# Kernel optimization log

Hardware: AMD Instinct MI355X
Metric: run time of the kernel (lower is better)

Reference implementation:

```python
import jax, jax.numpy as jnp
import numpy as np

D_MODEL = 3072
N_HEADS = 24
HEAD_DIM = D_MODEL // N_HEADS          # 128
Q_PROJ = D_MODEL // 2                  # 1536
KV_PROJ = 2 * D_MODEL // 3             # 2048
ROPE_DIM = HEAD_DIM // 2               # 64 (qk_rope_dim == qk_no_rope_dim)
MAX_LEN = 2048
ROPE_THETA = 10000.0
EPS = 1e-6
B, S = 2, 2048


def setup_inputs() -> dict:
    key = jax.random.key(0)
    ks = jax.random.split(key, 7)
    return {
        "x": jax.random.normal(ks[0], (B, S, D_MODEL), dtype=jnp.float32),
        "scale": jnp.ones((D_MODEL,), dtype=jnp.float32),
        "w_dq": 0.01 * jax.random.normal(ks[1], (D_MODEL, Q_PROJ), dtype=jnp.float32),
        "w_uq": 0.01 * jax.random.normal(ks[2], (Q_PROJ, D_MODEL), dtype=jnp.float32),
        "w_dkv": 0.01 * jax.random.normal(ks[3], (D_MODEL, KV_PROJ + ROPE_DIM), dtype=jnp.float32),
        "w_ukv": 0.01 * jax.random.normal(ks[4], (KV_PROJ, D_MODEL + N_HEADS * ROPE_DIM), dtype=jnp.float32),
        "w_o": 0.01 * jax.random.normal(ks[5], (D_MODEL, D_MODEL), dtype=jnp.float32),
    }


def _rope_cos_sin(seq_len):
    # freqs over full head_dim, sliced to rope_dim//2 then tiled x2 (as in torch repeat)
    freqs = 1.0 / (ROPE_THETA ** (jnp.arange(0, HEAD_DIM, 2, dtype=jnp.float32) / HEAD_DIM))
    angles = jnp.arange(seq_len, dtype=jnp.float32)[:, None] * freqs[None, :]  # [S, 64]
    ang = angles[:, : ROPE_DIM // 2]                                            # [S, 32]
    cos = jnp.tile(jnp.cos(ang), (1, 2))                                        # [S, 64]
    sin = jnp.tile(jnp.sin(ang), (1, 2))
    return cos[None, None], sin[None, None]  # [1,1,S,64]


def _rotate_half(t):
    a, b = jnp.split(t, 2, axis=-1)
    return jnp.concatenate([-b, a], axis=-1)


def reference(x, scale, w_dq, w_uq, w_dkv, w_ukv, w_o):
    b, s, _ = x.shape
    # RMSNorm pre-normalization
    xn = scale * (x * jax.lax.rsqrt(jnp.mean(x * x, axis=-1, keepdims=True) + EPS))
    # two-stage query projection
    q = (xn @ w_dq) @ w_uq                                   # [B,S,D]
    q = q.reshape(b, s, N_HEADS, HEAD_DIM).transpose(0, 2, 1, 3)  # [B,H,S,hd]
    q_no_rope, q_rope = jnp.split(q, [ROPE_DIM], axis=-1)
    cos, sin = _rope_cos_sin(s)
    q_rope = q_rope * cos + _rotate_half(q_rope) * sin
    # KV down projection (this is the kv cache)
    kv_down = xn @ w_dkv                                     # [B,S,KV_PROJ+rope]
    kv_no_rope, k_rope = jnp.split(kv_down, [KV_PROJ], axis=-1)
    # KV up projection
    kv_up = kv_no_rope @ w_ukv                               # [B,S,H*(hd+rope)]
    kv_up = kv_up.reshape(b, s, N_HEADS, HEAD_DIM + ROPE_DIM).transpose(0, 2, 1, 3)
    key, value = jnp.split(kv_up, [ROPE_DIM], axis=-1)       # key [B,H,S,64], value [B,H,S,128]
    # shared rope key (one head, broadcast to all heads)
    k_rope = k_rope[:, None, :, :]                           # [B,1,S,64]
    k_rope = k_rope * cos + _rotate_half(k_rope) * sin
    k_rope = jnp.broadcast_to(k_rope, (b, N_HEADS, s, ROPE_DIM))
    final_q = jnp.concatenate([q_no_rope, q_rope], axis=-1)  # [B,H,S,128]
    final_k = jnp.concatenate([key, k_rope], axis=-1)        # [B,H,S,128]
    # masked SDPA (causal, past_length=0)
    inv_scale = 1.0 / jnp.sqrt(jnp.asarray(HEAD_DIM, dtype=x.dtype))
    scores = jnp.einsum("bhsd,bhtd->bhst", final_q, final_k) * inv_scale
    causal = jnp.tril(jnp.ones((s, s), dtype=bool))
    scores = jnp.where(causal[None, None], scores, jnp.asarray(-1e30, dtype=scores.dtype))
    attn = jax.nn.softmax(scores, axis=-1)
    attn_out = jnp.einsum("bhst,bhtd->bhsd", attn, value)    # [B,H,S,128]
    attn_out = attn_out.transpose(0, 2, 1, 3).reshape(b, s, D_MODEL)
    output = attn_out @ w_o.T
    return output, kv_down
```

## Files before the change

### kernel.cpp

```cpp
#include <hip/hip_runtime.h>
#include <hip/hip_bf16.h>
#include <stdint.h>

using bf16_t = __bf16;
using bf16x8 = __attribute__((ext_vector_type(8))) __bf16;
using bf16x4 = __attribute__((ext_vector_type(4))) __bf16;
using f32x4  = __attribute__((ext_vector_type(4))) float;

#define D_MODEL 3072
#define N_HEADS 24
#define HEAD_DIM 128
#define Q_PROJ 1536
#define KV_PROJ 2048
#define ROPE_DIM 64
#define S_LEN 2048
#define NTOK 4096
#define KVDN 2112
#define KVUN 4608

__device__ __forceinline__ void async_ld16(const void* g, void* l) {
    __builtin_amdgcn_global_load_lds(
        (__attribute__((address_space(1))) uint32_t*)(uintptr_t)g,
        (__attribute__((address_space(3))) uint32_t*)(uint32_t)(uintptr_t)l,
        16, 0, 0);
}

#define BARRIER() __builtin_amdgcn_s_barrier()
#define WAITVN(n) asm volatile("s_waitcnt vmcnt(" #n ")" ::: "memory")

__global__ __launch_bounds__(256) void rmsnorm_kernel(
    const float* __restrict__ x, const float* __restrict__ sc, bf16_t* __restrict__ xn)
{
    const int tok = blockIdx.x;
    const int t = threadIdx.x;
    const float4* xr = (const float4*)(x + (size_t)tok * D_MODEL);
    float4 a = xr[t], b = xr[t + 256], c = xr[t + 512];
    float ss = a.x*a.x + a.y*a.y + a.z*a.z + a.w*a.w
             + b.x*b.x + b.y*b.y + b.z*b.z + b.w*b.w
             + c.x*c.x + c.y*c.y + c.z*c.z + c.w*c.w;
    #pragma unroll
    for (int off = 32; off >= 1; off >>= 1) ss += __shfl_xor(ss, off);
    __shared__ float red[4];
    if ((t & 63) == 0) red[t >> 6] = ss;
    __syncthreads();
    const float inv = rsqrtf((red[0] + red[1] + red[2] + red[3]) * (1.0f / D_MODEL) + 1e-6f);
    const float4* sr = (const float4*)sc;
    float4 s0 = sr[t], s1 = sr[t + 256], s2 = sr[t + 512];
    bf16x4* xo = (bf16x4*)(xn + (size_t)tok * D_MODEL);
    bf16x4 o;
    o[0]=(bf16_t)(a.x*s0.x*inv); o[1]=(bf16_t)(a.y*s0.y*inv); o[2]=(bf16_t)(a.z*s0.z*inv); o[3]=(bf16_t)(a.w*s0.w*inv);
    xo[t] = o;
    o[0]=(bf16_t)(b.x*s1.x*inv); o[1]=(bf16_t)(b.y*s1.y*inv); o[2]=(bf16_t)(b.z*s1.z*inv); o[3]=(bf16_t)(b.w*s1.w*inv);
    xo[t + 256] = o;
    o[0]=(bf16_t)(c.x*s2.x*inv); o[1]=(bf16_t)(c.y*s2.y*inv); o[2]=(bf16_t)(c.z*s2.z*inv); o[3]=(bf16_t)(c.w*s2.w*inv);
    xo[t + 512] = o;
}

__global__ void transpose_conv(const float* __restrict__ in, bf16_t* __restrict__ out, int K, int N)
{
    __shared__ float tile[32][33];
    const int n0 = blockIdx.x * 32, k0 = blockIdx.y * 32;
    const int tx = threadIdx.x, ty = threadIdx.y;
    #pragma unroll
    for (int i = 0; i < 32; i += 8)
        tile[ty + i][tx] = in[(size_t)(k0 + ty + i) * N + n0 + tx];
    __syncthreads();
    #pragma unroll
    for (int i = 0; i < 32; i += 8)
        out[(size_t)(n0 + ty + i) * K + k0 + tx] = (bf16_t)tile[tx][ty + i];
}

__global__ void conv_bf16(const float* __restrict__ in, bf16_t* __restrict__ out, int n4)
{
    const int stride = gridDim.x * 256;
    for (int i = blockIdx.x * 256 + threadIdx.x; i < n4; i += stride) {
        float4 v = ((const float4*)in)[i];
        bf16x4 o;
        o[0] = (bf16_t)v.x; o[1] = (bf16_t)v.y; o[2] = (bf16_t)v.z; o[3] = (bf16_t)v.w;
        ((bf16x4*)out)[i] = o;
    }
}

template<int RH, int BNF>
__device__ __forceinline__ void mfmaQ(f32x4 (&acc)[8][BNF], const bf16x8 (&af)[4],
                                      const bf16x8 (&bfv)[BNF]) {
    __builtin_amdgcn_s_setprio(1);
    #pragma unroll
    for (int i = 0; i < 4; ++i)
        #pragma unroll
        for (int cf = 0; cf < BNF; ++cf)
            acc[RH*4+i][cf] = __builtin_amdgcn_mfma_f32_16x16x32_bf16(af[i], bfv[cf], acc[RH*4+i][cf], 0, 0, 0);
    __builtin_amdgcn_s_setprio(0);
}

template<int BNF>
__global__ __launch_bounds__(512, 2) void gemm256(
    const bf16_t* __restrict__ A, const bf16_t* __restrict__ B, int N, int K,
    float* __restrict__ Cf, int ldf, int flo, int fhi,
    bf16_t* __restrict__ Cb1, int ldb1, int b1lo, int b1hi,
    bf16_t* __restrict__ Cb2, int ldb2, int b2lo, int b2hi,
    bf16_t* __restrict__ vt, float cbscale)
{
    constexpr int BN = BNF * 64;
    constexpr uint32_t BSLOT = BNF * 4096;
    __shared__ char LDS[65536 + 4 * BSLOT];
    char* Lc = LDS;
    const int tid = threadIdx.x;
    const int wv = tid >> 6, lane = tid & 63;
    const int fr = lane & 15, fg = lane >> 4;
    const int wr = wv >> 2, wc = wv & 3;
    const bool bwave = (wv < 2 * BNF);

    int lin = blockIdx.y * gridDim.x + blockIdx.x;
    const int nwg = gridDim.x * gridDim.y;
    if ((nwg & 7) == 0) lin = (lin & 7) * (nwg >> 3) + (lin >> 3);
    const int bx = lin % gridDim.x, by = lin / gridDim.x;
    const int m0 = by << 8, n0 = bx * BN;

    const uint32_t slot4 = (uint32_t)((fg ^ ((fr >> 1) & 3)) << 4);

    const bf16_t* agp[2]; const bf16_t* bgp[2];
    uint32_t aoff[2], boff[2];
    #pragma unroll
    for (int j = 0; j < 2; ++j) {
        const int c = j * 512 + tid;
        const int g = c ^ ((c >> 3) & 3);
        agp[j] = A + (size_t)(m0 + (g >> 2)) * K + (g & 3) * 8;
        aoff[j] = (uint32_t)((j * 8 + wv) * 1024);
        const int cb = j * (BNF * 128) + tid;
        const int gb = cb ^ ((cb >> 3) & 3);
        int br = n0 + (gb >> 2); if (br > N - 1) br = N - 1;
        bgp[j] = B + (size_t)br * K + (gb & 3) * 8;
        boff[j] = (uint32_t)(j * (BNF * 2048) + wv * 1024);
    }

    f32x4 acc[8][BNF];
    f32x4 zero = {0.f, 0.f, 0.f, 0.f};
    #pragma unroll
    for (int i = 0; i < 8; ++i)
        #pragma unroll
        for (int j = 0; j < BNF; ++j) acc[i][j] = zero;

    bf16x8 A0[4], A1[4], B0[BNF], B1[BNF];
    const int rowA = (wr << 7) + fr;
    const int rowB = wc * (BNF * 16) + fr;

    auto stA = [&](int t, int kh) {
        const uint32_t sb = (uint32_t)(((2*t + kh) & 3) << 14);
        #pragma unroll
        for (int j = 0; j < 2; ++j)
            async_ld16(agp[j] + t * 64 + kh * 32, Lc + sb + aoff[j]);
    };
    auto stB = [&](int t, int kh) {
        const uint32_t sb = 65536u + (uint32_t)(((2*t + kh) & 3) * BSLOT);
        if (tid < BNF * 128) {
            #pragma unroll
            for (int j = 0; j < 2; ++j)
                async_ld16(bgp[j] + t * 64 + kh * 32, Lc + sb + boff[j]);
        }
    };
    auto ldA4 = [&](int t, int kh, int rh, bf16x8 (&dst)[4]) {
        const uint32_t base = (uint32_t)(((2*t + kh) & 3) << 14);
        #pragma unroll
        for (int i = 0; i < 4; ++i)
            dst[i] = *(const bf16x8*)(Lc + base + (rowA + (rh * 4 + i) * 16) * 64 + slot4);
    };
    auto ldBn = [&](int t, int kh, bf16x8 (&dst)[BNF]) {
        const uint32_t base = 65536u + (uint32_t)(((2*t + kh) & 3) * BSLOT);
        #pragma unroll
        for (int cf = 0; cf < BNF; ++cf)
            dst[cf] = *(const bf16x8*)(Lc + base + (rowB + cf * 16) * 64 + slot4);
    };

    const int NT = K >> 6;
    stA(0, 0); stB(0, 0); stA(0, 1); stB(0, 1);
    stA(1, 0); stB(1, 0); stA(1, 1); stB(1, 1);
    if (bwave) { WAITVN(8); } else { WAITVN(4); }
    BARRIER();
    ldA4(0, 0, 0, A0); ldBn(0, 0, B0);

    for (int t = 0; t < NT; ++t) {
        const bool pref = (t + 2 < NT);
        ldA4(t, 0, 1, A1);
        mfmaQ<0, BNF>(acc, A0, B0);
        if (pref) { if (bwave) { WAITVN(4); } else { WAITVN(2); } }
        else      { WAITVN(0); }
        BARRIER();
        ldA4(t, 1, 0, A0); ldBn(t, 1, B1);
        if (pref) { stA(t + 2, 0); stB(t + 2, 0); }
        mfmaQ<1, BNF>(acc, A1, B0);
        BARRIER();
        ldA4(t, 1, 1, A1);
        mfmaQ<0, BNF>(acc, A0, B1);
        BARRIER();
        if (t + 1 < NT) { ldA4(t + 1, 0, 0, A0); ldBn(t + 1, 0, B0); }
        if (pref) { stA(t + 2, 1); stB(t + 2, 1); }
        mfmaQ<1, BNF>(acc, A1, B1);
        BARRIER();
    }

    const int colb = n0 + wc * (BNF * 16) + fr;
    const int rowb = m0 + (wr << 7) + fg * 4;
    if (vt) {
        #pragma unroll
        for (int rf = 0; rf < 8; ++rf) {
            const int row0 = rowb + rf * 16;
            const int bb = row0 >> 11, s0 = row0 & 2047;
            #pragma unroll
            for (int cf = 0; cf < BNF; ++cf) {
                const int col = colb + cf * 16;
                const int h = col / 192;
                const int dm = col - h * 192;
                if (dm < 64) {
                    #pragma unroll
                    for (int r = 0; r < 4; ++r)
                        Cb1[(size_t)(row0 + r) * ldb1 + col] = (bf16_t)acc[rf][cf][r];
                } else {
                    bf16x4 o;
                    o[0] = (bf16_t)acc[rf][cf][0];
                    o[1] = (bf16_t)acc[rf][cf][1];
                    o[2] = (bf16_t)acc[rf][cf][2];
                    o[3] = (bf16_t)acc[rf][cf][3];
                    *(bf16x4*)(vt + ((size_t)((bb * 24 + h) * 128 + dm - 64)) * 2048 + s0) = o;
                }
            }
        }
    } else {
        #pragma unroll
        for (int rf = 0; rf < 8; ++rf)
            #pragma unroll
            for (int cf = 0; cf < BNF; ++cf) {
                const int col = colb + cf * 16;
                #pragma unroll
                for (int r = 0; r < 4; ++r) {
                    const int row = rowb + rf * 16 + r;
                    const float v = acc[rf][cf][r];
                    if (Cf  && col >= flo  && col < fhi)  Cf [(size_t)row * ldf  + col - flo]  = v;
                    if (Cb1 && col >= b1lo && col < b1hi) Cb1[(size_t)row * ldb1 + col - b1lo] = (bf16_t)(v * cbscale);
                    if (Cb2 && col >= b2lo && col < b2hi) Cb2[(size_t)row * ldb2 + col - b2lo] = (bf16_t)v;
                }
            }
    }
}

__global__ void rope_tab(float* __restrict__ ctab, float* __restrict__ stab)
{
    const int idx = blockIdx.x * 256 + threadIdx.x;
    if (idx >= S_LEN * 32) return;
    const int s = idx >> 5, i = idx & 31;
    const float freq = powf(10000.0f, -(float)(2 * i) * (1.0f / 128.0f));
    const float ang = (float)s * freq;
    ctab[idx] = cosf(ang);
    stab[idx] = sinf(ang);
}

__global__ void rope_q_kernel(bf16_t* __restrict__ q, const float* __restrict__ ctab,
                              const float* __restrict__ stab)
{
    const int idx = blockIdx.x * 256 + threadIdx.x;
    if (idx >= NTOK * N_HEADS * 32) return;
    const int i = idx & 31;
    const int rest = idx >> 5;
    const int h = rest % N_HEADS;
    const int tok = rest / N_HEADS;
    const int s = tok & (S_LEN - 1);
    bf16_t* p = q + (size_t)tok * D_MODEL + h * HEAD_DIM + 64;
    const float a = (float)p[i], b = (float)p[i + 32];
    const float c = ctab[s * 32 + i], sn = stab[s * 32 + i];
    p[i]      = (bf16_t)(a * c - b * sn);
    p[i + 32] = (bf16_t)(b * c + a * sn);
}

__global__ void rope_k_kernel(const float* __restrict__ kvd, bf16_t* __restrict__ kr,
                              const float* __restrict__ ctab, const float* __restrict__ stab)
{
    const int idx = blockIdx.x * 256 + threadIdx.x;
    if (idx >= NTOK * 32) return;
    const int i = idx & 31;
    const int tok = idx >> 5;
    const int s = tok & (S_LEN - 1);
    const float* p = kvd + (size_t)tok * KVDN + KV_PROJ;
    const float a = p[i], b = p[i + 32];
    const float c = ctab[s * 32 + i], sn = stab[s * 32 + i];
    kr[(size_t)tok * 64 + i]      = (bf16_t)(a * c - b * sn);
    kr[(size_t)tok * 64 + i + 32] = (bf16_t)(b * c + a * sn);
}

__global__ __launch_bounds__(256, 2) void attn_fwd(
    const bf16_t* __restrict__ Q, const bf16_t* __restrict__ KVUP,
    const bf16_t* __restrict__ KR, const bf16_t* __restrict__ VT,
    bf16_t* __restrict__ AO)
{
    __shared__ bf16_t Knr[2][64 * 64];
    __shared__ bf16_t Krp[2][64 * 64];
    __shared__ bf16_t Vls[2][128 * 64];

    const int bh = blockIdx.y;
    const int b = bh / N_HEADS, h = bh % N_HEADS;
    const int wave = threadIdx.x >> 6, lane = threadIdx.x & 63;
    const int fr = lane & 15, fg = lane >> 4;
    const int rx = fr & 7;
    const int hi = fg >> 1;
    const int s0l = fr + 32 * (fg & 1);
    const int s1l = s0l + 16;

    const bf16_t* Kb  = KVUP + (size_t)b * S_LEN * KVUN + (size_t)h * 192;
    const bf16_t* KRb = KR + (size_t)b * S_LEN * 64;
    const bf16_t* Vb  = VT + (size_t)bh * HEAD_DIM * S_LEN;

    const int srow   = lane >> 3;
    const int schunk = (lane & 7) ^ srow;

    f32x4 zero = {0.f, 0.f, 0.f, 0.f};

    #pragma unroll 1
    for (int tp = 0; tp < 2; ++tp) {
        const int qt = (tp == 0) ? blockIdx.x : (15 - blockIdx.x);
        const int qb = qt * 128;
        const int wrow0 = qb + wave * 32;

        bf16x8 qf[2][4];
        #pragma unroll
        for (int rf = 0; rf < 2; ++rf)
            #pragma unroll
            for (int kc = 0; kc < 4; ++kc)
                qf[rf][kc] = *(const bf16x8*)(Q + (size_t)(b * S_LEN + wrow0 + rf * 16 + fr) * D_MODEL
                                              + h * HEAD_DIM + kc * 32 + fg * 8);
        f32x4 oacc[2][8];
        float m_i[2], l_i[2];
        #pragma unroll
        for (int rf = 0; rf < 2; ++rf) {
            #pragma unroll
            for (int nf = 0; nf < 8; ++nf) oacc[rf][nf] = zero;
            m_i[rf] = -1e30f; l_i[rf] = 0.f;
        }

        auto stage = [&](int kvb, int bf) {
            #pragma unroll
            for (int c = 0; c < 2; ++c) {
                const int r0 = wave * 16 + c * 8;
                async_ld16(Kb  + (size_t)(kvb + r0 + srow) * KVUN + schunk * 8, &Knr[bf][r0 * 64]);
                async_ld16(KRb + (size_t)(kvb + r0 + srow) * 64   + schunk * 8, &Krp[bf][r0 * 64]);
            }
            #pragma unroll
            for (int c = 0; c < 4; ++c) {
                const int r0 = wave * 32 + c * 8;
                async_ld16(Vb + (size_t)(r0 + srow) * S_LEN + kvb + schunk * 8, &Vls[bf][r0 * 64]);
            }
        };

        const int kvend = qb + 128;
        int cur = 0;
        stage(0, 0);
        __syncthreads();

        #pragma unroll 1
        for (int kvb = 0; kvb < kvend; kvb += 64) {
            if (kvb + 64 < kvend) stage(kvb + 64, cur ^ 1);

            if (kvb <= wrow0 + 31) {
                const bf16_t* Kc = Knr[cur];
                const bf16_t* Rc = Krp[cur];
                const bf16_t* Vc = Vls[cur];

                f32x4 sacc[2][4];
                #pragma unroll
                for (int rf = 0; rf < 2; ++rf)
                    #pragma unroll
                    for (int jn = 0; jn < 4; ++jn) sacc[rf][jn] = zero;
                __builtin_amdgcn_s_setprio(1);
                #pragma unroll
                for (int jn = 0; jn < 4; ++jn) {
                    const int krow = jn * 16 + fr;
                    bf16x8 kA = *(const bf16x8*)(Kc + krow * 64 + (((0 + fg) ^ rx) << 3));
                    bf16x8 kB = *(const bf16x8*)(Kc + krow * 64 + (((4 + fg) ^ rx) << 3));
                    bf16x8 kC = *(const bf16x8*)(Rc + krow * 64 + (((0 + fg) ^ rx) << 3));
                    bf16x8 kD = *(const bf16x8*)(Rc + krow * 64 + (((4 + fg) ^ rx) << 3));
                    #pragma unroll
                    for (int rf = 0; rf < 2; ++rf) {
                        sacc[rf][jn] = __builtin_amdgcn_mfma_f32_16x16x32_bf16(kA, qf[rf][0], sacc[rf][jn], 0, 0, 0);
                        sacc[rf][jn] = __builtin_amdgcn_mfma_f32_16x16x32_bf16(kB, qf[rf][1], sacc[rf][jn], 0, 0, 0);
                        sacc[rf][jn] = __builtin_amdgcn_mfma_f32_16x16x32_bf16(kC, qf[rf][2], sacc[rf][jn], 0, 0, 0);
                        sacc[rf][jn] = __builtin_amdgcn_mfma_f32_16x16x32_bf16(kD, qf[rf][3], sacc[rf][jn], 0, 0, 0);
                    }
                }
                __builtin_amdgcn_s_setprio(0);

                const bool needMask = (kvb + 63 > wrow0);
                uint32_t pk[2][4][2];
                #pragma unroll
                for (int rf = 0; rf < 2; ++rf) {
                    const int qrow = wrow0 + rf * 16 + fr;
                    float mx = -1e30f;
                    #pragma unroll
                    for (int jn = 0; jn < 4; ++jn)
                        #pragma unroll
                        for (int r = 0; r < 4; ++r) {
                            float v = sacc[rf][jn][r];
                            if (needMask && (kvb + jn * 16 + fg * 4 + r > qrow)) v = -1e30f;
                            sacc[rf][jn][r] = v;
                            mx = fmaxf(mx, v);
                        }
                    mx = fmaxf(mx, __shfl_xor(mx, 16));
                    mx = fmaxf(mx, __shfl_xor(mx, 32));
                    if (!__all(mx <= m_i[rf] + 8.f)) {
                        const float mn = fmaxf(m_i[rf], mx);
                        const float sc = __builtin_amdgcn_exp2f(m_i[rf] - mn);
                        m_i[rf] = mn;
                        l_i[rf] *= sc;
                        #pragma unroll
                        for (int nf = 0; nf < 8; ++nf)
                            #pragma unroll
                            for (int r = 0; r < 4; ++r) oacc[rf][nf][r] *= sc;
                    }
                    const float mn = m_i[rf];
                    float ls = 0.f;
                    #pragma unroll
                    for (int jn = 0; jn < 4; ++jn) {
                        float p0 = __builtin_amdgcn_exp2f(sacc[rf][jn][0] - mn);
                        float p1 = __builtin_amdgcn_exp2f(sacc[rf][jn][1] - mn);
                        float p2 = __builtin_amdgcn_exp2f(sacc[rf][jn][2] - mn);
                        float p3 = __builtin_amdgcn_exp2f(sacc[rf][jn][3] - mn);
                        ls += (p0 + p1) + (p2 + p3);
                        union { bf16x4 h; uint32_t w[2]; } cv;
                        cv.h[0] = (bf16_t)p0; cv.h[1] = (bf16_t)p1;
                        cv.h[2] = (bf16_t)p2; cv.h[3] = (bf16_t)p3;
                        pk[rf][jn][0] = cv.w[0]; pk[rf][jn][1] = cv.w[1];
                    }
                    ls += __shfl_xor(ls, 16);
                    ls += __shfl_xor(ls, 32);
                    l_i[rf] += ls;
                }

                bf16x8 bfr[2][2];
                #pragma unroll
                for (int rf = 0; rf < 2; ++rf)
                    #pragma unroll
                    for (int ks = 0; ks < 2; ++ks) {
                        const uint32_t t00 = __shfl(pk[rf][2*ks][0],   s0l);
                        const uint32_t t01 = __shfl(pk[rf][2*ks][1],   s0l);
                        const uint32_t t10 = __shfl(pk[rf][2*ks+1][0], s0l);
                        const uint32_t t11 = __shfl(pk[rf][2*ks+1][1], s0l);
                        const uint32_t u00 = __shfl(pk[rf][2*ks][0],   s1l);
                        const uint32_t u01 = __shfl(pk[rf][2*ks][1],   s1l);
                        const uint32_t u10 = __shfl(pk[rf][2*ks+1][0], s1l);
                        const uint32_t u11 = __shfl(pk[rf][2*ks+1][1], s1l);
                        union { bf16x8 h; uint32_t w[4]; } bb;
                        bb.w[0] = hi ? t10 : t00;
                        bb.w[1] = hi ? t11 : t01;
                        bb.w[2] = hi ? u10 : u00;
                        bb.w[3] = hi ? u11 : u01;
                        bfr[rf][ks] = bb.h;
                    }

                __builtin_amdgcn_s_setprio(1);
                #pragma unroll
                for (int nf = 0; nf < 8; ++nf) {
                    const int vrow = nf * 16 + fr;
                    bf16x8 v0 = *(const bf16x8*)(Vc + vrow * 64 + (((0 + fg) ^ rx) << 3));
                    bf16x8 v1 = *(const bf16x8*)(Vc + vrow * 64 + (((4 + fg) ^ rx) << 3));
                    #pragma unroll
                    for (int rf = 0; rf < 2; ++rf) {
                        oacc[rf][nf] = __builtin_amdgcn_mfma_f32_16x16x32_bf16(v0, bfr[rf][0], oacc[rf][nf], 0, 0, 0);
                        oacc[rf][nf] = __builtin_amdgcn_mfma_f32_16x16x32_bf16(v1, bfr[rf][1], oacc[rf][nf], 0, 0, 0);
                    }
                }
                __builtin_amdgcn_s_setprio(0);
            }
            __syncthreads();
            cur ^= 1;
        }

        #pragma unroll
        for (int rf = 0; rf < 2; ++rf) {
            const float rl = __builtin_amdgcn_rcpf(l_i[rf]);
            const int qrow = wrow0 + rf * 16 + fr;
            bf16_t* aob = AO + (size_t)(b * S_LEN + qrow) * D_MODEL + h * HEAD_DIM + fg * 4;
            #pragma unroll
            for (int nf = 0; nf < 8; ++nf) {
                bf16x4 o;
                o[0] = (bf16_t)(oacc[rf][nf][0] * rl);
                o[1] = (bf16_t)(oacc[rf][nf][1] * rl);
                o[2] = (bf16_t)(oacc[rf][nf][2] * rl);
                o[3] = (bf16_t)(oacc[rf][nf][3] * rl);
                *(bf16x4*)(aob + nf * 16) = o;
            }
        }
    }
}

extern "C" void kernel_launch(void* const* d_in, const int* in_sizes, int n_in,
                              void* d_out, int out_size, void* d_ws, size_t ws_size,
                              hipStream_t stream)
{
    const float* x     = (const float*)d_in[0];
    const float* scale = (const float*)d_in[1];
    const float* w_dq  = (const float*)d_in[2];
    const float* w_uq  = (const float*)d_in[3];
    const float* w_dkv = (const float*)d_in[4];
    const float* w_ukv = (const float*)d_in[5];
    const float* w_o   = (const float*)d_in[6];
    float* out0 = (float*)d_out;
    float* out1 = out0 + (size_t)NTOK * D_MODEL;

    if (ws_size < 187039744ull) return;
    char* ws = (char*)d_ws;
    bf16_t* XN    = (bf16_t*)(ws + 0);
    bf16_t* WCAT  = (bf16_t*)(ws + 25165824ull);
    bf16_t* WUQT  = (bf16_t*)(ws + 47579136ull);
    bf16_t* WUKVT = (bf16_t*)(ws + 57016320ull);
    bf16_t* WOB   = (bf16_t*)(ws + 75890688ull);
    bf16_t* QD    = (bf16_t*)(ws + 94765056ull);
    bf16_t* Qb    = (bf16_t*)(ws + 107347968ull);
    bf16_t* KVNR  = (bf16_t*)(ws + 132513792ull);
    bf16_t* KVUP  = (bf16_t*)(ws + 149291008ull);
    bf16_t* KRB   = (bf16_t*)(ws + 94765056ull);
    float*  CTAB  = (float*) (ws + 95289344ull);
    float*  STAB  = (float*) (ws + 95551488ull);
    bf16_t* VTb   = WCAT;
    bf16_t* AO    = XN;

    const float l2e_isc = 0.127500625f;

    rmsnorm_kernel<<<NTOK, 256, 0, stream>>>(x, scale, XN);
    transpose_conv<<<dim3(1536/32, 3072/32), dim3(32,8), 0, stream>>>(w_dq,  WCAT, 3072, 1536);
    transpose_conv<<<dim3(2112/32, 3072/32), dim3(32,8), 0, stream>>>(w_dkv, WCAT + (size_t)1536*3072, 3072, 2112);
    transpose_conv<<<dim3(3072/32, 1536/32), dim3(32,8), 0, stream>>>(w_uq,  WUQT, 1536, 3072);
    transpose_conv<<<dim3(4608/32, 2048/32), dim3(32,8), 0, stream>>>(w_ukv, WUKVT, 2048, 4608);
    conv_bf16<<<2048, 256, 0, stream>>>(w_o, WOB, (D_MODEL * D_MODEL) / 4);

    gemm256<4><<<dim3(15, 16), 512, 0, stream>>>(XN, WCAT, 3648, 3072,
        out1, KVDN, 1536, 3648,
        QD,   Q_PROJ, 0, 1536,
        KVNR, KV_PROJ, 1536, 3584, nullptr, 1.0f);
    gemm256<3><<<dim3(16, 16), 512, 0, stream>>>(QD, WUQT, 3072, 1536,
        nullptr, 0, 0, 0, Qb, D_MODEL, 0, 3072, nullptr, 0, 0, 0, nullptr, l2e_isc);
    rope_tab<<<(S_LEN * 32 + 255) / 256, 256, 0, stream>>>(CTAB, STAB);
    rope_q_kernel<<<(NTOK * N_HEADS * 32 + 255) / 256, 256, 0, stream>>>(Qb, CTAB, STAB);
    rope_k_kernel<<<(NTOK * 32 + 255) / 256, 256, 0, stream>>>(out1, KRB, CTAB, STAB);
    gemm256<3><<<dim3(24, 16), 512, 0, stream>>>(KVNR, WUKVT, 4608, 2048,
        nullptr, 0, 0, 0, KVUP, KVUN, 0, 0, nullptr, 0, 0, 0, VTb, 1.0f);
    attn_fwd<<<dim3(8, 48), 256, 0, stream>>>(Qb, KVUP, KRB, VTb, AO);
    gemm256<3><<<dim3(16, 16), 512, 0, stream>>>(AO, WOB, 3072, 3072,
        out0, D_MODEL, 0, 3072, nullptr, 0, 0, 0, nullptr, 0, 0, 0, nullptr, 1.0f);
}
```

Baseline: 521.7 us.

## Drop LDS staging in attention; load K/V fragments directly from global per wave

The attention kernel no longer stages K, rope-K and V tiles into double-buffered shared memory with async loads and block barriers. Each wave now reads its MFMA operands straight from global memory (through the cache) and runs only up to its own causal end, so the __syncthreads and LDS traffic go away. Launch bounds are raised to 4 blocks per CU. The trade-off is that the four waves of a block, which share the same K/V rows, each fetch them from global/L2 separately, and there is no explicit prefetch overlap, so load latency sits on the critical path.

```diff
diff --git a/kernel.cpp b/kernel.cpp
--- a/kernel.cpp
+++ b/kernel.cpp
@@ -286,20 +286,15 @@
     kr[(size_t)tok * 64 + i + 32] = (bf16_t)(b * c + a * sn);
 }
 
-__global__ __launch_bounds__(256, 2) void attn_fwd(
+__global__ __launch_bounds__(256, 4) void attn_fwd(
     const bf16_t* __restrict__ Q, const bf16_t* __restrict__ KVUP,
     const bf16_t* __restrict__ KR, const bf16_t* __restrict__ VT,
     bf16_t* __restrict__ AO)
 {
-    __shared__ bf16_t Knr[2][64 * 64];
-    __shared__ bf16_t Krp[2][64 * 64];
-    __shared__ bf16_t Vls[2][128 * 64];
-
     const int bh = blockIdx.y;
     const int b = bh / N_HEADS, h = bh % N_HEADS;
     const int wave = threadIdx.x >> 6, lane = threadIdx.x & 63;
     const int fr = lane & 15, fg = lane >> 4;
-    const int rx = fr & 7;
     const int hi = fg >> 1;
     const int s0l = fr + 32 * (fg & 1);
     const int s1l = s0l + 16;
@@ -307,9 +302,6 @@
     const bf16_t* Kb  = KVUP + (size_t)b * S_LEN * KVUN + (size_t)h * 192;
     const bf16_t* KRb = KR + (size_t)b * S_LEN * 64;
     const bf16_t* Vb  = VT + (size_t)bh * HEAD_DIM * S_LEN;
-
-    const int srow   = lane >> 3;
-    const int schunk = (lane & 7) ^ srow;
 
     f32x4 zero = {0.f, 0.f, 0.f, 0.f};
 
@@ -335,140 +327,114 @@
             m_i[rf] = -1e30f; l_i[rf] = 0.f;
         }
 
-        auto stage = [&](int kvb, int bf) {
-            #pragma unroll
-            for (int c = 0; c < 2; ++c) {
-                const int r0 = wave * 16 + c * 8;
-                async_ld16(Kb  + (size_t)(kvb + r0 + srow) * KVUN + schunk * 8, &Knr[bf][r0 * 64]);
-                async_ld16(KRb + (size_t)(kvb + r0 + srow) * 64   + schunk * 8, &Krp[bf][r0 * 64]);
+        const int kvend_w = wrow0 + 32;
+        #pragma unroll 1
+        for (int kvb = 0; kvb < kvend_w; kvb += 64) {
+            f32x4 sacc[2][4];
+            #pragma unroll
+            for (int rf = 0; rf < 2; ++rf)
+                #pragma unroll
+                for (int jn = 0; jn < 4; ++jn) sacc[rf][jn] = zero;
+            __builtin_amdgcn_s_setprio(1);
+            #pragma unroll
+            for (int jn = 0; jn < 4; ++jn) {
+                const int krow = kvb + jn * 16 + fr;
+                const bf16_t* kp = Kb + (size_t)krow * KVUN + fg * 8;
+                const bf16_t* rp = KRb + (size_t)krow * 64 + fg * 8;
+                bf16x8 kA = *(const bf16x8*)(kp);
+                bf16x8 kB = *(const bf16x8*)(kp + 32);
+                bf16x8 kC = *(const bf16x8*)(rp);
+                bf16x8 kD = *(const bf16x8*)(rp + 32);
+                #pragma unroll
+                for (int rf = 0; rf < 2; ++rf) {
+                    sacc[rf][jn] = __builtin_amdgcn_mfma_f32_16x16x32_bf16(kA, qf[rf][0], sacc[rf][jn], 0, 0, 0);
+                    sacc[rf][jn] = __builtin_amdgcn_mfma_f32_16x16x32_bf16(kB, qf[rf][1], sacc[rf][jn], 0, 0, 0);
+                    sacc[rf][jn] = __builtin_amdgcn_mfma_f32_16x16x32_bf16(kC, qf[rf][2], sacc[rf][jn], 0, 0, 0);
+                    sacc[rf][jn] = __builtin_amdgcn_mfma_f32_16x16x32_bf16(kD, qf[rf][3], sacc[rf][jn], 0, 0, 0);
+                }
             }
-            #pragma unroll
-            for (int c = 0; c < 4; ++c) {
-                const int r0 = wave * 32 + c * 8;
-                async_ld16(Vb + (size_t)(r0 + srow) * S_LEN + kvb + schunk * 8, &Vls[bf][r0 * 64]);
+            __builtin_amdgcn_s_setprio(0);
+
+            const bool needMask = (kvb + 63 > wrow0);
+            uint32_t pk[2][4][2];
+            #pragma unroll
+            for (int rf = 0; rf < 2; ++rf) {
+                const int qrow = wrow0 + rf * 16 + fr;
+                float mx = -1e30f;
+                #pragma unroll
+                for (int jn = 0; jn < 4; ++jn)
+                    #pragma unroll
+                    for (int r = 0; r < 4; ++r) {
+                        float v = sacc[rf][jn][r];
+                        if (needMask && (kvb + jn * 16 + fg * 4 + r > qrow)) v = -1e30f;
+                        sacc[rf][jn][r] = v;
+                        mx = fmaxf(mx, v);
+                    }
+                mx = fmaxf(mx, __shfl_xor(mx, 16));
+                mx = fmaxf(mx, __shfl_xor(mx, 32));
+                if (!__all(mx <= m_i[rf] + 8.f)) {
+                    const float mn = fmaxf(m_i[rf], mx);
+                    const float sc = __builtin_amdgcn_exp2f(m_i[rf] - mn);
+                    m_i[rf] = mn;
+                    l_i[rf] *= sc;
+                    #pragma unroll
+                    for (int nf = 0; nf < 8; ++nf)
+                        #pragma unroll
+                        for (int r = 0; r < 4; ++r) oacc[rf][nf][r] *= sc;
+                }
+                const float mn = m_i[rf];
+                float ls = 0.f;
+                #pragma unroll
+                for (int jn = 0; jn < 4; ++jn) {
+                    float p0 = __builtin_amdgcn_exp2f(sacc[rf][jn][0] - mn);
+                    float p1 = __builtin_amdgcn_exp2f(sacc[rf][jn][1] - mn);
+                    float p2 = __builtin_amdgcn_exp2f(sacc[rf][jn][2] - mn);
+                    float p3 = __builtin_amdgcn_exp2f(sacc[rf][jn][3] - mn);
+                    ls += (p0 + p1) + (p2 + p3);
+                    union { bf16x4 h; uint32_t w[2]; } cv;
+                    cv.h[0] = (bf16_t)p0; cv.h[1] = (bf16_t)p1;
+                    cv.h[2] = (bf16_t)p2; cv.h[3] = (bf16_t)p3;
+                    pk[rf][jn][0] = cv.w[0]; pk[rf][jn][1] = cv.w[1];
+                }
+                ls += __shfl_xor(ls, 16);
+                ls += __shfl_xor(ls, 32);
+                l_i[rf] += ls;
             }
-        };
-
-        const int kvend = qb + 128;
-        int cur = 0;
-        stage(0, 0);
-        __syncthreads();
-
-        #pragma unroll 1
-        for (int kvb = 0; kvb < kvend; kvb += 64) {
-            if (kvb + 64 < kvend) stage(kvb + 64, cur ^ 1);
-
-            if (kvb <= wrow0 + 31) {
-                const bf16_t* Kc = Knr[cur];
-                const bf16_t* Rc = Krp[cur];
-                const bf16_t* Vc = Vls[cur];
-
-                f32x4 sacc[2][4];
-                #pragma unroll
-                for (int rf = 0; rf < 2; ++rf)
-                    #pragma unroll
-                    for (int jn = 0; jn < 4; ++jn) sacc[rf][jn] = zero;
-                __builtin_amdgcn_s_setprio(1);
-                #pragma unroll
-                for (int jn = 0; jn < 4; ++jn) {
-                    const int krow = jn * 16 + fr;
-                    bf16x8 kA = *(const bf16x8*)(Kc + krow * 64 + (((0 + fg) ^ rx) << 3));
-                    bf16x8 kB = *(const bf16x8*)(Kc + krow * 64 + (((4 + fg) ^ rx) << 3));
-                    bf16x8 kC = *(const bf16x8*)(Rc + krow * 64 + (((0 + fg) ^ rx) << 3));
-                    bf16x8 kD = *(const bf16x8*)(Rc + krow * 64 + (((4 + fg) ^ rx) << 3));
-                    #pragma unroll
-                    for (int rf = 0; rf < 2; ++rf) {
-                        sacc[rf][jn] = __builtin_amdgcn_mfma_f32_16x16x32_bf16(kA, qf[rf][0], sacc[rf][jn], 0, 0, 0);
-                        sacc[rf][jn] = __builtin_amdgcn_mfma_f32_16x16x32_bf16(kB, qf[rf][1], sacc[rf][jn], 0, 0, 0);
-                        sacc[rf][jn] = __builtin_amdgcn_mfma_f32_16x16x32_bf16(kC, qf[rf][2], sacc[rf][jn], 0, 0, 0);
-                        sacc[rf][jn] = __builtin_amdgcn_mfma_f32_16x16x32_bf16(kD, qf[rf][3], sacc[rf][jn], 0, 0, 0);
-                    }
-                }
-                __builtin_amdgcn_s_setprio(0);
-
-                const bool needMask = (kvb + 63 > wrow0);
-                uint32_t pk[2][4][2];
+
+            bf16x8 bfr[2][2];
+            #pragma unroll
+            for (int rf = 0; rf < 2; ++rf)
+                #pragma unroll
+                for (int ks = 0; ks < 2; ++ks) {
+                    const uint32_t t00 = __shfl(pk[rf][2*ks][0],   s0l);
+                    const uint32_t t01 = __shfl(pk[rf][2*ks][1],   s0l);
+                    const uint32_t t10 = __shfl(pk[rf][2*ks+1][0], s0l);
+                    const uint32_t t11 = __shfl(pk[rf][2*ks+1][1], s0l);
+                    const uint32_t u00 = __shfl(pk[rf][2*ks][0],   s1l);
+                    const uint32_t u01 = __shfl(pk[rf][2*ks][1],   s1l);
+                    const uint32_t u10 = __shfl(pk[rf][2*ks+1][0], s1l);
+                    const uint32_t u11 = __shfl(pk[rf][2*ks+1][1], s1l);
+                    union { bf16x8 h; uint32_t w[4]; } bb;
+                    bb.w[0] = hi ? t10 : t00;
+                    bb.w[1] = hi ? t11 : t01;
+                    bb.w[2] = hi ? u10 : u00;
+                    bb.w[3] = hi ? u11 : u01;
+                    bfr[rf][ks] = bb.h;
+                }
+
+            __builtin_amdgcn_s_setprio(1);
+            #pragma unroll
+            for (int nf = 0; nf < 8; ++nf) {
+                const bf16_t* vp = Vb + (size_t)(nf * 16 + fr) * S_LEN + kvb + fg * 8;
+                bf16x8 v0 = *(const bf16x8*)(vp);
+                bf16x8 v1 = *(const bf16x8*)(vp + 32);
                 #pragma unroll
                 for (int rf = 0; rf < 2; ++rf) {
-                    const int qrow = wrow0 + rf * 16 + fr;
-                    float mx = -1e30f;
-                    #pragma unroll
-                    for (int jn = 0; jn < 4; ++jn)
-                        #pragma unroll
-                        for (int r = 0; r < 4; ++r) {
-                            float v = sacc[rf][jn][r];
-                            if (needMask && (kvb + jn * 16 + fg * 4 + r > qrow)) v = -1e30f;
-                            sacc[rf][jn][r] = v;
-                            mx = fmaxf(mx, v);
-                        }
-                    mx = fmaxf(mx, __shfl_xor(mx, 16));
-                    mx = fmaxf(mx, __shfl_xor(mx, 32));
-                    if (!__all(mx <= m_i[rf] + 8.f)) {
-                        const float mn = fmaxf(m_i[rf], mx);
-                        const float sc = __builtin_amdgcn_exp2f(m_i[rf] - mn);
-                        m_i[rf] = mn;
-                        l_i[rf] *= sc;
-                        #pragma unroll
-                        for (int nf = 0; nf < 8; ++nf)
-                            #pragma unroll
-                            for (int r = 0; r < 4; ++r) oacc[rf][nf][r] *= sc;
-                    }
-                    const float mn = m_i[rf];
-                    float ls = 0.f;
-                    #pragma unroll
-                    for (int jn = 0; jn < 4; ++jn) {
-                        float p0 = __builtin_amdgcn_exp2f(sacc[rf][jn][0] - mn);
-                        float p1 = __builtin_amdgcn_exp2f(sacc[rf][jn][1] - mn);
-                        float p2 = __builtin_amdgcn_exp2f(sacc[rf][jn][2] - mn);
-                        float p3 = __builtin_amdgcn_exp2f(sacc[rf][jn][3] - mn);
-                        ls += (p0 + p1) + (p2 + p3);
-                        union { bf16x4 h; uint32_t w[2]; } cv;
-                        cv.h[0] = (bf16_t)p0; cv.h[1] = (bf16_t)p1;
-                        cv.h[2] = (bf16_t)p2; cv.h[3] = (bf16_t)p3;
-                        pk[rf][jn][0] = cv.w[0]; pk[rf][jn][1] = cv.w[1];
-                    }
-                    ls += __shfl_xor(ls, 16);
-                    ls += __shfl_xor(ls, 32);
-                    l_i[rf] += ls;
-                }
-
-                bf16x8 bfr[2][2];
-                #pragma unroll
-                for (int rf = 0; rf < 2; ++rf)
-                    #pragma unroll
-                    for (int ks = 0; ks < 2; ++ks) {
-                        const uint32_t t00 = __shfl(pk[rf][2*ks][0],   s0l);
-                        const uint32_t t01 = __shfl(pk[rf][2*ks][1],   s0l);
-                        const uint32_t t10 = __shfl(pk[rf][2*ks+1][0], s0l);
-                        const uint32_t t11 = __shfl(pk[rf][2*ks+1][1], s0l);
-                        const uint32_t u00 = __shfl(pk[rf][2*ks][0],   s1l);
-                        const uint32_t u01 = __shfl(pk[rf][2*ks][1],   s1l);
-                        const uint32_t u10 = __shfl(pk[rf][2*ks+1][0], s1l);
-                        const uint32_t u11 = __shfl(pk[rf][2*ks+1][1], s1l);
-                        union { bf16x8 h; uint32_t w[4]; } bb;
-                        bb.w[0] = hi ? t10 : t00;
-                        bb.w[1] = hi ? t11 : t01;
-                        bb.w[2] = hi ? u10 : u00;
-                        bb.w[3] = hi ? u11 : u01;
-                        bfr[rf][ks] = bb.h;
-                    }
-
-                __builtin_amdgcn_s_setprio(1);
-                #pragma unroll
-                for (int nf = 0; nf < 8; ++nf) {
-                    const int vrow = nf * 16 + fr;
-                    bf16x8 v0 = *(const bf16x8*)(Vc + vrow * 64 + (((0 + fg) ^ rx) << 3));
-                    bf16x8 v1 = *(const bf16x8*)(Vc + vrow * 64 + (((4 + fg) ^ rx) << 3));
-                    #pragma unroll
-                    for (int rf = 0; rf < 2; ++rf) {
-                        oacc[rf][nf] = __builtin_amdgcn_mfma_f32_16x16x32_bf16(v0, bfr[rf][0], oacc[rf][nf], 0, 0, 0);
-                        oacc[rf][nf] = __builtin_amdgcn_mfma_f32_16x16x32_bf16(v1, bfr[rf][1], oacc[rf][nf], 0, 0, 0);
-                    }
-                }
-                __builtin_amdgcn_s_setprio(0);
+                    oacc[rf][nf] = __builtin_amdgcn_mfma_f32_16x16x32_bf16(v0, bfr[rf][0], oacc[rf][nf], 0, 0, 0);
+                    oacc[rf][nf] = __builtin_amdgcn_mfma_f32_16x16x32_bf16(v1, bfr[rf][1], oacc[rf][nf], 0, 0, 0);
+                }
             }
-            __syncthreads();
-            cur ^= 1;
+            __builtin_amdgcn_s_setprio(0);
         }
 
         #pragma unroll
```

Result: slower. 865.8 us (+66.0%).
